# Optimization experiments

Hardware: AMD Instinct MI355X
Metric: run time of the kernel (lower is better)

The kernel has to match this reference:

```python
import jax, jax.numpy as jnp
import numpy as np

EPS = 1e-6
BASE_THETA = 10000.0


def setup_inputs() -> dict:
    key = jax.random.key(0)
    ks = jax.random.split(key, 6)
    S, E = 4096, 4096
    scale = 1.0 / np.sqrt(E)
    return {
        "x": jax.random.normal(ks[0], (S, E), dtype=jnp.float32),
        "w_q": jax.random.normal(ks[1], (E, E), dtype=jnp.float32) * scale,
        "w_k": jax.random.normal(ks[2], (E, E), dtype=jnp.float32) * scale,
        "w_v": jax.random.normal(ks[3], (E, E), dtype=jnp.float32) * scale,
        "w_out": jax.random.normal(ks[4], (E, E), dtype=jnp.float32) * scale,
        "scaling_factor": jax.random.uniform(ks[5], (E,), dtype=jnp.float32, minval=0.5, maxval=1.5),
    }


def _rope_apply(t, cos, sin):
    # t: (S, D) fp16; cos/sin: (S, D//2) fp16. Closed form of the per-position
    # block-diagonal 2x2 rotation matrix matmul in the original loop:
    # out[2j]   =  t[2j]*cos + t[2j+1]*sin
    # out[2j+1] = -t[2j]*sin + t[2j+1]*cos
    S, D = t.shape
    t2 = t.reshape(S, D // 2, 2)
    even, odd = t2[..., 0], t2[..., 1]
    out = jnp.stack([even * cos + odd * sin, -even * sin + odd * cos], axis=-1)
    return out.reshape(S, D)


def reference(x, w_q, w_k, w_v, w_out, scaling_factor):
    f16, f32 = jnp.float16, jnp.float32
    S, E = x.shape
    # __init__: q / q_inv / head rotations are identity; quantize = cast fp16 (scale 1).
    # q_inv * scaling_factor.view(1,-1) == diag(scaling_factor) -> row-scale weights.
    wq = (scaling_factor[:, None] * w_q).astype(f16)
    wk = (scaling_factor[:, None] * w_k).astype(f16)
    wv = (scaling_factor[:, None] * w_v).astype(f16)
    wo = w_out.astype(f16)

    # input @ identity; rms_norm in fp32
    xn = x * jax.lax.rsqrt(jnp.mean(x * x, axis=-1, keepdims=True) + EPS)
    xq = xn.astype(f16)

    # quantized matmuls: fp16 operands, fp32 accumulation, cast back to fp16
    q = (xq.astype(f32) @ wq.astype(f32)).astype(f16)
    k = (xq.astype(f32) @ wk.astype(f32)).astype(f16)
    v = (xq.astype(f32) @ wv.astype(f32)).astype(f16)

    # RoPE over full feature dim (size = E), vectorized over positions
    pos = jnp.arange(S, dtype=f32)[:, None]
    j = jnp.arange(E // 2, dtype=f32)[None, :]
    theta = pos / jnp.power(BASE_THETA, 2.0 * j / E)
    cos = jnp.cos(theta).astype(f16)
    sin = jnp.sin(theta).astype(f16)
    q = _rope_apply(q, cos, sin)
    k = _rope_apply(k, cos, sin)

    # rot_head_k_tiled is identity -> quantize is just fp16 cast (already fp16)
    scores = (q.astype(f32) @ k.T.astype(f32)).astype(f16)
    scores = scores / np.float16(np.sqrt(E))
    # causal mask: strict upper triangle -> -inf
    row = jnp.arange(S)[:, None]
    col = jnp.arange(S)[None, :]
    scores = jnp.where(col > row, jnp.float16(-jnp.inf), scores)
    attn_w = jax.nn.softmax(scores, axis=1)
    attn = attn_w @ v  # fp16 matmul as in original

    out = (attn.astype(f32) @ wo.astype(f32)).astype(f16)
    return out
```

## Files before the change

### kernel.cpp

```cpp
#include <hip/hip_runtime.h>
#include <hip/hip_bf16.h>
#include <cmath>


typedef _Float16 f16;
typedef _Float16 f16x4 __attribute__((ext_vector_type(4)));
typedef _Float16 f16x8 __attribute__((ext_vector_type(8)));
typedef float f32x4 __attribute__((ext_vector_type(4)));

#define S_DIM 4096
#define E_DIM 4096

__device__ __forceinline__ void gload_lds16(const void* g, void* l) {
  __builtin_amdgcn_global_load_lds((const __attribute__((address_space(1))) void*)g,
                                   (__attribute__((address_space(3))) void*)l,
                                   16, 0, 0);
}

__global__ __launch_bounds__(256) void rmsnorm_f16(const float* __restrict__ x,
                                                   f16* __restrict__ xq, int E) {
  const int row = blockIdx.x;
  const int t = threadIdx.x;
  const float4* xr = (const float4*)(x + (size_t)row * E);
  float4 v[4];
  float ss = 0.f;
#pragma unroll
  for (int i = 0; i < 4; ++i) {
    v[i] = xr[t + 256 * i];
    ss += v[i].x * v[i].x + v[i].y * v[i].y + v[i].z * v[i].z + v[i].w * v[i].w;
  }
#pragma unroll
  for (int o = 1; o < 64; o <<= 1) ss += __shfl_xor(ss, o);
  __shared__ float red[4];
  const int wid = t >> 6, lane = t & 63;
  if (lane == 0) red[wid] = ss;
  __syncthreads();
  const float tot = red[0] + red[1] + red[2] + red[3];
  const float r = 1.0f / sqrtf(tot / (float)E + 1e-6f);
  f16* xo = xq + (size_t)row * E;
#pragma unroll
  for (int i = 0; i < 4; ++i) {
    f16x4 o;
    o[0] = (f16)(v[i].x * r);
    o[1] = (f16)(v[i].y * r);
    o[2] = (f16)(v[i].z * r);
    o[3] = (f16)(v[i].w * r);
    *(f16x4*)(xo + 4 * (t + 256 * i)) = o;
  }
}

__global__ __launch_bounds__(256) void wconv_t(const float* __restrict__ W,
                                               const float* __restrict__ s,
                                               f16* __restrict__ WT, int N) {
  __shared__ f16 tile[64][65];
  const int tr = blockIdx.y * 64;
  const int tc = blockIdx.x * 64;
  const int t = threadIdx.x;
  const int r = t / 16;
  const int c4 = (t % 16) * 4;
#pragma unroll
  for (int i = 0; i < 4; ++i) {
    const int row = r + i * 16;
    float4 w = *(const float4*)(W + (size_t)(tr + row) * N + tc + c4);
    const float sc = s ? s[tr + row] : 1.0f;
    tile[row][c4 + 0] = (f16)(w.x * sc);
    tile[row][c4 + 1] = (f16)(w.y * sc);
    tile[row][c4 + 2] = (f16)(w.z * sc);
    tile[row][c4 + 3] = (f16)(w.w * sc);
  }
  __syncthreads();
#pragma unroll
  for (int i = 0; i < 4; ++i) {
    const int row = r + i * 16;
    f16x4 o;
    o[0] = tile[c4 + 0][row];
    o[1] = tile[c4 + 1][row];
    o[2] = tile[c4 + 2][row];
    o[3] = tile[c4 + 3][row];
    *(f16x4*)(WT + (size_t)(tc + row) * N + tr + c4) = o;
  }
}

__global__ __launch_bounds__(256) void freq_tab_k(float* __restrict__ tab) {
  const int j = blockIdx.x * 256 + threadIdx.x;
  if (j < 2048) tab[j] = (float)pow(10000.0, (double)j / 2048.0);
}

__global__ __launch_bounds__(256) void rope_qk(f16* __restrict__ q,
                                               f16* __restrict__ k,
                                               const float* __restrict__ ftab,
                                               int E) {
  const int idx = blockIdx.x * 256 + threadIdx.x;
  const int cpr = E / 8;
  const int pos = idx / cpr;
  const int ch = idx % cpr;
  const int j0 = ch * 4;
  const float fpos = (float)pos;
  f16x8 qv = *(f16x8*)(q + (size_t)idx * 8);
  f16x8 kv = *(f16x8*)(k + (size_t)idx * 8);
  f16x8 qo, ko;
#pragma unroll
  for (int p = 0; p < 4; ++p) {
    const int j = j0 + p;
    const float th = fpos / ftab[j];
    float sn, cs;
    sincosf(th, &sn, &cs);
    const f16 c16 = (f16)cs, s16 = (f16)sn;
    const float c = (float)c16, s = (float)s16;
    {
      const float e = (float)qv[2 * p], o = (float)qv[2 * p + 1];
      const f16 t1 = (f16)(e * c), t2 = (f16)(o * s);
      const f16 u1 = (f16)(-(e * s)), u2 = (f16)(o * c);
      qo[2 * p] = (f16)((float)t1 + (float)t2);
      qo[2 * p + 1] = (f16)((float)u1 + (float)u2);
    }
    {
      const float e = (float)kv[2 * p], o = (float)kv[2 * p + 1];
      const f16 t1 = (f16)(e * c), t2 = (f16)(o * s);
      const f16 u1 = (f16)(-(e * s)), u2 = (f16)(o * c);
      ko[2 * p] = (f16)((float)t1 + (float)t2);
      ko[2 * p + 1] = (f16)((float)u1 + (float)u2);
    }
  }
  *(f16x8*)(q + (size_t)idx * 8) = qo;
  *(f16x8*)(k + (size_t)idx * 8) = ko;
}

__global__ __launch_bounds__(256) void softmax_causal(f16* __restrict__ sc, int S) {
  const int row = blockIdx.x;
  const int t = threadIdx.x;
  f16* p = sc + (size_t)row * S;
  float v[16];
  bool msk[16];
#pragma unroll
  for (int i = 0; i < 2; ++i) {
    f16x8 a = *(const f16x8*)(p + (size_t)(i * 256 + t) * 8);
#pragma unroll
    for (int j = 0; j < 8; ++j) v[i * 8 + j] = (float)a[j];
  }
  float m = -1e30f;
#pragma unroll
  for (int i = 0; i < 2; ++i)
#pragma unroll
    for (int j = 0; j < 8; ++j) {
      const int col = (i * 256 + t) * 8 + j;
      const int ii = i * 8 + j;
      msk[ii] = (col > row);
      if (!msk[ii]) m = fmaxf(m, v[ii]);
    }
#pragma unroll
  for (int o = 1; o < 64; o <<= 1) m = fmaxf(m, __shfl_xor(m, o));
  __shared__ float red[4];
  const int wid = t >> 6, lane = t & 63;
  if (lane == 0) red[wid] = m;
  __syncthreads();
  m = fmaxf(fmaxf(red[0], red[1]), fmaxf(red[2], red[3]));
  __syncthreads();
  f16 e16[16];
  float sum = 0.f;
#pragma unroll
  for (int i = 0; i < 16; ++i) {
    if (msk[i]) {
      e16[i] = (f16)0.0f;
    } else {
      const f16 d16 = (f16)(v[i] - m);
      e16[i] = (f16)expf((float)d16);
      sum += (float)e16[i];
    }
  }
#pragma unroll
  for (int o = 1; o < 64; o <<= 1) sum += __shfl_xor(sum, o);
  if (lane == 0) red[wid] = sum;
  __syncthreads();
  sum = red[0] + red[1] + red[2] + red[3];
  const f16 den16 = (f16)sum;
  const float den = (float)den16;
#pragma unroll
  for (int i = 0; i < 2; ++i) {
    f16x8 o;
#pragma unroll
    for (int j = 0; j < 8; ++j) {
      const int ii = i * 8 + j;
      o[j] = msk[ii] ? (f16)0.0f : (f16)((float)e16[ii] / den);
    }
    *(f16x8*)(p + (size_t)(i * 256 + t) * 8) = o;
  }
}

__device__ __forceinline__ void store_out(f16* p, f16 v) { *p = v; }
__device__ __forceinline__ void store_out(float* p, f16 v) { *p = (float)v; }

template <typename OUT, int MODE>
__global__ __launch_bounds__(512, 2) void gemm256(const f16* __restrict__ A,
                                                  const f16* __restrict__ BT,
                                                  OUT* __restrict__ C,
                                                  int M, int N, int K, float alpha) {
  if (MODE == 1 && blockIdx.x > blockIdx.y) return;
  const int bm = blockIdx.y * 256, bn = blockIdx.x * 256;
  const int kend = (MODE == 2) ? (bm + 256 < K ? bm + 256 : K) : K;
  const int nt = kend >> 6;

  extern __shared__ char smem[];
  f16(*lds)[2][256][64] = (f16(*)[2][256][64])smem;

  const int tid = threadIdx.x;
  const int lane = tid & 63;
  const int wid = tid >> 6;
  const int wr = wid >> 2;
  const int wc = wid & 3;
  const f16* Ab = A + (size_t)bm * K;
  const f16* Bb = BT + (size_t)bn * K;

  const int l8 = lane >> 3;
  const int gxor8 = ((lane & 7) ^ l8) * 8;
  const int lr = lane & 15;
  const int shi = lane >> 4;
  const int rsw = lr & 7;

  auto STAGE_P = [&](int p) {
    const int c = p + 6;
    const int Ts = c >> 2, hh = c & 3;
    if (Ts >= nt) return;
    const int k0 = Ts << 6;
    const int bsel = Ts & 1;
#pragma unroll
    for (int l = 0; l < 2; ++l) {
      const int rih0 = wid * 16 + l * 8;
      if (hh == 0 || hh == 3) {
        const int row0 = (rih0 & 63) + ((rih0 >> 6) << 7) + ((hh == 3) ? 64 : 0);
        gload_lds16(Ab + (size_t)(row0 + l8) * K + k0 + gxor8,
                    &lds[bsel][0][row0][0]);
      } else {
        const int row0 = (rih0 & 31) + ((rih0 >> 5) << 6) + ((hh == 2) ? 32 : 0);
        gload_lds16(Bb + (size_t)(row0 + l8) * K + k0 + gxor8,
                    &lds[bsel][1][row0][0]);
      }
    }
  };

  f32x4 acc[8][4] = {};
  f16x8 afr0[4][2], afr1[4][2], b0r[2][2], b1r[2][2];

#pragma unroll
  for (int p = -6; p < 0; ++p) STAGE_P(p);

  for (int T = 0; T < nt; ++T) {
    const int cur = T & 1;
    __builtin_amdgcn_sched_barrier(0);
    if (T + 1 < nt) {
      asm volatile("s_waitcnt vmcnt(4)" ::: "memory");
    } else {
      asm volatile("s_waitcnt vmcnt(0)" ::: "memory");
    }
    __builtin_amdgcn_sched_barrier(0);
    __builtin_amdgcn_s_barrier();
    __builtin_amdgcn_sched_barrier(0);
#pragma unroll
    for (int m2 = 0; m2 < 4; ++m2)
#pragma unroll
      for (int kk = 0; kk < 2; ++kk)
        afr0[m2][kk] = *(const f16x8*)&lds[cur][0][wr * 128 + m2 * 16 + lr]
                                          [((kk * 4 + shi) ^ rsw) * 8];
#pragma unroll
    for (int n2 = 0; n2 < 2; ++n2)
#pragma unroll
      for (int kk = 0; kk < 2; ++kk)
        b0r[n2][kk] = *(const f16x8*)&lds[cur][1][wc * 64 + n2 * 16 + lr]
                                         [((kk * 4 + shi) ^ rsw) * 8];
    STAGE_P(4 * T);
    __builtin_amdgcn_sched_barrier(0);
    if (T > 0) {
      __builtin_amdgcn_s_setprio(1);
#pragma unroll
      for (int m2 = 0; m2 < 4; ++m2)
#pragma unroll
        for (int n2 = 0; n2 < 2; ++n2)
#pragma unroll
          for (int kk = 0; kk < 2; ++kk)
            acc[4 + m2][2 + n2] = __builtin_amdgcn_mfma_f32_16x16x32_f16(
                afr1[m2][kk], b1r[n2][kk], acc[4 + m2][2 + n2], 0, 0, 0);
      __builtin_amdgcn_s_setprio(0);
    }
    __builtin_amdgcn_sched_barrier(0);
#pragma unroll
    for (int n2 = 0; n2 < 2; ++n2)
#pragma unroll
      for (int kk = 0; kk < 2; ++kk)
        b1r[n2][kk] = *(const f16x8*)&lds[cur][1][wc * 64 + 32 + n2 * 16 + lr]
                                         [((kk * 4 + shi) ^ rsw) * 8];
    STAGE_P(4 * T + 1);
    __builtin_amdgcn_sched_barrier(0);
    __builtin_amdgcn_s_setprio(1);
#pragma unroll
    for (int m2 = 0; m2 < 4; ++m2)
#pragma unroll
      for (int n2 = 0; n2 < 2; ++n2)
#pragma unroll
        for (int kk = 0; kk < 2; ++kk)
          acc[m2][n2] = __builtin_amdgcn_mfma_f32_16x16x32_f16(
              afr0[m2][kk], b0r[n2][kk], acc[m2][n2], 0, 0, 0);
    __builtin_amdgcn_s_setprio(0);
    __builtin_amdgcn_sched_barrier(0);
    __builtin_amdgcn_s_barrier();
    __builtin_amdgcn_sched_barrier(0);
#pragma unroll
    for (int m2 = 0; m2 < 4; ++m2)
#pragma unroll
      for (int kk = 0; kk < 2; ++kk)
        afr1[m2][kk] = *(const f16x8*)&lds[cur][0][wr * 128 + 64 + m2 * 16 + lr]
                                          [((kk * 4 + shi) ^ rsw) * 8];
    STAGE_P(4 * T + 2);
    __builtin_amdgcn_sched_barrier(0);
    __builtin_amdgcn_s_setprio(1);
#pragma unroll
    for (int m2 = 0; m2 < 4; ++m2)
#pragma unroll
      for (int n2 = 0; n2 < 2; ++n2)
#pragma unroll
        for (int kk = 0; kk < 2; ++kk)
          acc[m2][2 + n2] = __builtin_amdgcn_mfma_f32_16x16x32_f16(
              afr0[m2][kk], b1r[n2][kk], acc[m2][2 + n2], 0, 0, 0);
    __builtin_amdgcn_s_setprio(0);
    __builtin_amdgcn_sched_barrier(0);
    STAGE_P(4 * T + 3);
    __builtin_amdgcn_sched_barrier(0);
    __builtin_amdgcn_s_setprio(1);
#pragma unroll
    for (int m2 = 0; m2 < 4; ++m2)
#pragma unroll
      for (int n2 = 0; n2 < 2; ++n2)
#pragma unroll
        for (int kk = 0; kk < 2; ++kk)
          acc[4 + m2][n2] = __builtin_amdgcn_mfma_f32_16x16x32_f16(
              afr1[m2][kk], b0r[n2][kk], acc[4 + m2][n2], 0, 0, 0);
    __builtin_amdgcn_s_setprio(0);
  }
  __builtin_amdgcn_s_setprio(1);
#pragma unroll
  for (int m2 = 0; m2 < 4; ++m2)
#pragma unroll
    for (int n2 = 0; n2 < 2; ++n2)
#pragma unroll
      for (int kk = 0; kk < 2; ++kk)
        acc[4 + m2][2 + n2] = __builtin_amdgcn_mfma_f32_16x16x32_f16(
            afr1[m2][kk], b1r[n2][kk], acc[4 + m2][2 + n2], 0, 0, 0);
  __builtin_amdgcn_s_setprio(0);

  const int rb_l = wr * 128 + (lane >> 4) * 4;
  const int cb_l = wc * 64 + (lane & 15);

  if (MODE == 4) {
    f16* tl = (f16*)smem;
    asm volatile("s_waitcnt lgkmcnt(0)" ::: "memory");
    __builtin_amdgcn_s_barrier();
#pragma unroll
    for (int mm = 0; mm < 8; ++mm)
#pragma unroll
      for (int nn = 0; nn < 4; ++nn) {
        const int c = cb_l + nn * 16;
#pragma unroll
        for (int r = 0; r < 4; ++r)
          tl[(size_t)c * 258 + rb_l + mm * 16 + r] = (f16)acc[mm][nn][r];
      }
    asm volatile("s_waitcnt lgkmcnt(0)" ::: "memory");
    __builtin_amdgcn_s_barrier();
    const int c = tid >> 1, hf = tid & 1;
#pragma unroll
    for (int i = 0; i < 16; ++i) {
      f16x8 v8 = *(const f16x8*)&tl[(size_t)c * 258 + hf * 128 + i * 8];
      *(f16x8*)((f16*)C + (size_t)(bn + c) * M + bm + hf * 128 + i * 8) = v8;
    }
    return;
  }

#pragma unroll
  for (int mm = 0; mm < 8; ++mm)
#pragma unroll
    for (int nn = 0; nn < 4; ++nn) {
      const int col = bn + cb_l + nn * 16;
#pragma unroll
      for (int r = 0; r < 4; ++r) {
        f16 h = (f16)acc[mm][nn][r];
        if (alpha != 1.0f) h = (f16)((float)h * alpha);
        store_out(&C[(size_t)(bm + rb_l + mm * 16 + r) * N + col], h);
      }
    }
}

extern "C" void kernel_launch(void* const* d_in, const int* in_sizes, int n_in,
                              void* d_out, int out_size, void* d_ws, size_t ws_size,
                              hipStream_t stream) {
  const float* x = (const float*)d_in[0];
  const float* wq = (const float*)d_in[1];
  const float* wk = (const float*)d_in[2];
  const float* wv = (const float*)d_in[3];
  const float* wo = (const float*)d_in[4];
  const float* sf = (const float*)d_in[5];
  float* out = (float*)d_out;

  const int S = S_DIM, E = E_DIM;
  const size_t U = (size_t)S * E * sizeof(f16);
  char* ws = (char*)d_ws;
  f16* xq = (f16*)(ws + 0 * U);
  f16* wT = (f16*)(ws + 1 * U);
  f16* q  = (f16*)(ws + 2 * U);
  f16* k  = (f16*)(ws + 3 * U);
  f16* vT = (f16*)d_out;

  const int LDSA = 131072;
  const int LDSB = 135168;
  hipFuncSetAttribute(reinterpret_cast<const void*>(&gemm256<f16, 0>),
                      hipFuncAttributeMaxDynamicSharedMemorySize, LDSA);
  hipFuncSetAttribute(reinterpret_cast<const void*>(&gemm256<f16, 1>),
                      hipFuncAttributeMaxDynamicSharedMemorySize, LDSA);
  hipFuncSetAttribute(reinterpret_cast<const void*>(&gemm256<f16, 2>),
                      hipFuncAttributeMaxDynamicSharedMemorySize, LDSA);
  hipFuncSetAttribute(reinterpret_cast<const void*>(&gemm256<f16, 4>),
                      hipFuncAttributeMaxDynamicSharedMemorySize, LDSB);
  hipFuncSetAttribute(reinterpret_cast<const void*>(&gemm256<float, 0>),
                      hipFuncAttributeMaxDynamicSharedMemorySize, LDSA);

  dim3 b256(256), b512(512);
  dim3 gT(E / 64, E / 64);
  dim3 gG(E / 256, S / 256);

  rmsnorm_f16<<<S, b256, 0, stream>>>(x, xq, E);

  wconv_t<<<gT, b256, 0, stream>>>(wq, sf, wT, E);
  gemm256<f16, 0><<<gG, b512, LDSA, stream>>>(xq, wT, q, S, E, E, 1.0f);
  wconv_t<<<gT, b256, 0, stream>>>(wk, sf, wT, E);
  gemm256<f16, 0><<<gG, b512, LDSA, stream>>>(xq, wT, k, S, E, E, 1.0f);
  wconv_t<<<gT, b256, 0, stream>>>(wv, sf, wT, E);
  gemm256<f16, 4><<<gG, b512, LDSB, stream>>>(xq, wT, vT, S, E, E, 1.0f);

  float* ftab = (float*)wT;
  freq_tab_k<<<8, b256, 0, stream>>>(ftab);
  rope_qk<<<(S * (E / 8)) / 256, b256, 0, stream>>>(q, k, ftab, E);

  f16* sc = wT;
  gemm256<f16, 1><<<dim3(S / 256, S / 256), b512, LDSA, stream>>>(q, k, sc, S, S,
                                                                  E, 1.0f / 64.0f);
  softmax_causal<<<S, b256, 0, stream>>>(sc, S);

  f16* attn = q;
  gemm256<f16, 2><<<gG, b512, LDSA, stream>>>(sc, vT, attn, S, E, S, 1.0f);

  f16* wT2 = k;
  wconv_t<<<gT, b256, 0, stream>>>(wo, (const float*)nullptr, wT2, E);
  gemm256<float, 0><<<gG, b512, LDSA, stream>>>(attn, wT2, out, S, E, E, 1.0f);
}
```

Before: 792.8 us.

## Unroll GEMM main loop by two with precomputed load pointers; trim causal softmax range

The GEMM main loop is rewritten as a templated per-tile step unrolled twice. Buffer indices become compile-time constants and global load addresses are precomputed pointers advanced by 64 each step, replacing the per-stage lambda's branchy index arithmetic. The causal softmax now skips loading, exponentiating and storing columns past the row's 256-aligned block, which the causal GEMM leaves unwritten. This assumes nt is even and at least 2, and leaves the skipped softmax columns as whatever the score buffer already holds.

```diff
diff --git a/kernel.cpp b/kernel.cpp
--- a/kernel.cpp
+++ b/kernel.cpp
@@ -130,24 +130,30 @@
   const int row = blockIdx.x;
   const int t = threadIdx.x;
   f16* p = sc + (size_t)row * S;
+  const int cend = (row & ~255) + 256;
   float v[16];
   bool msk[16];
+  bool act[2];
 #pragma unroll
   for (int i = 0; i < 2; ++i) {
-    f16x8 a = *(const f16x8*)(p + (size_t)(i * 256 + t) * 8);
-#pragma unroll
-    for (int j = 0; j < 8; ++j) v[i * 8 + j] = (float)a[j];
+    act[i] = ((i * 256 + t) * 8) < cend;
+    if (act[i]) {
+      f16x8 a = *(const f16x8*)(p + (size_t)(i * 256 + t) * 8);
+#pragma unroll
+      for (int j = 0; j < 8; ++j) v[i * 8 + j] = (float)a[j];
+    }
   }
   float m = -1e30f;
 #pragma unroll
   for (int i = 0; i < 2; ++i)
-#pragma unroll
-    for (int j = 0; j < 8; ++j) {
-      const int col = (i * 256 + t) * 8 + j;
-      const int ii = i * 8 + j;
-      msk[ii] = (col > row);
-      if (!msk[ii]) m = fmaxf(m, v[ii]);
-    }
+    if (act[i])
+#pragma unroll
+      for (int j = 0; j < 8; ++j) {
+        const int col = (i * 256 + t) * 8 + j;
+        const int ii = i * 8 + j;
+        msk[ii] = (col > row);
+        if (!msk[ii]) m = fmaxf(m, v[ii]);
+      }
 #pragma unroll
   for (int o = 1; o < 64; o <<= 1) m = fmaxf(m, __shfl_xor(m, o));
   __shared__ float red[4];
@@ -159,15 +165,19 @@
   f16 e16[16];
   float sum = 0.f;
 #pragma unroll
-  for (int i = 0; i < 16; ++i) {
-    if (msk[i]) {
-      e16[i] = (f16)0.0f;
-    } else {
-      const f16 d16 = (f16)(v[i] - m);
-      e16[i] = (f16)expf((float)d16);
-      sum += (float)e16[i];
-    }
-  }
+  for (int i = 0; i < 2; ++i)
+    if (act[i])
+#pragma unroll
+      for (int j = 0; j < 8; ++j) {
+        const int ii = i * 8 + j;
+        if (msk[ii]) {
+          e16[ii] = (f16)0.0f;
+        } else {
+          const f16 d16 = (f16)(v[ii] - m);
+          e16[ii] = (f16)expf((float)d16);
+          sum += (float)e16[ii];
+        }
+      }
 #pragma unroll
   for (int o = 1; o < 64; o <<= 1) sum += __shfl_xor(sum, o);
   if (lane == 0) red[wid] = sum;
@@ -177,6 +187,7 @@
   const float den = (float)den16;
 #pragma unroll
   for (int i = 0; i < 2; ++i) {
+    if (!act[i]) continue;
     f16x8 o;
 #pragma unroll
     for (int j = 0; j < 8; ++j) {
@@ -189,6 +200,121 @@
 
 __device__ __forceinline__ void store_out(f16* p, f16 v) { *p = v; }
 __device__ __forceinline__ void store_out(float* p, f16 v) { *p = (float)v; }
+
+#define MFMA_H __builtin_amdgcn_mfma_f32_16x16x32_f16
+
+template <int CURX, bool S01, bool S23, bool LASTV>
+__device__ __forceinline__ void tile_one(
+    f16 (*lds)[2][256][64], bool tailv, f32x4 (&acc)[8][4],
+    f16x8 (&afr0)[4][2], f16x8 (&afr1)[4][2], f16x8 (&b0r)[2][2],
+    f16x8 (&b1r)[2][2],
+    const f16*& gB2a, const f16*& gB2b, const f16*& gA3a, const f16*& gA3b,
+    const f16*& gA0a, const f16*& gA0b, const f16*& gB1a, const f16*& gB1b,
+    f16* dB2a, f16* dB2b, f16* dA3a, f16* dA3b,
+    f16* dA0a, f16* dA0b, f16* dB1a, f16* dB1b,
+    int wr, int wc, int lr, int shi, int rsw) {
+  __builtin_amdgcn_sched_barrier(0);
+  if (LASTV) {
+    asm volatile("s_waitcnt vmcnt(0)" ::: "memory");
+  } else {
+    asm volatile("s_waitcnt vmcnt(4)" ::: "memory");
+  }
+  __builtin_amdgcn_sched_barrier(0);
+  __builtin_amdgcn_s_barrier();
+  __builtin_amdgcn_sched_barrier(0);
+#pragma unroll
+  for (int m2 = 0; m2 < 4; ++m2)
+#pragma unroll
+    for (int kk = 0; kk < 2; ++kk)
+      afr0[m2][kk] = *(const f16x8*)&lds[CURX][0][wr * 128 + m2 * 16 + lr]
+                                        [((kk * 4 + shi) ^ rsw) * 8];
+#pragma unroll
+  for (int n2 = 0; n2 < 2; ++n2)
+#pragma unroll
+    for (int kk = 0; kk < 2; ++kk)
+      b0r[n2][kk] = *(const f16x8*)&lds[CURX][1][wc * 64 + n2 * 16 + lr]
+                                       [((kk * 4 + shi) ^ rsw) * 8];
+  if (S01) {
+    gload_lds16(gB2a, dB2a);
+    gload_lds16(gB2b, dB2b);
+  }
+  __builtin_amdgcn_sched_barrier(0);
+  if (tailv) {
+    __builtin_amdgcn_s_setprio(1);
+#pragma unroll
+    for (int m2 = 0; m2 < 4; ++m2)
+#pragma unroll
+      for (int n2 = 0; n2 < 2; ++n2)
+#pragma unroll
+        for (int kk = 0; kk < 2; ++kk)
+          acc[4 + m2][2 + n2] =
+              MFMA_H(afr1[m2][kk], b1r[n2][kk], acc[4 + m2][2 + n2], 0, 0, 0);
+    __builtin_amdgcn_s_setprio(0);
+  }
+  __builtin_amdgcn_sched_barrier(0);
+#pragma unroll
+  for (int n2 = 0; n2 < 2; ++n2)
+#pragma unroll
+    for (int kk = 0; kk < 2; ++kk)
+      b1r[n2][kk] = *(const f16x8*)&lds[CURX][1][wc * 64 + 32 + n2 * 16 + lr]
+                                       [((kk * 4 + shi) ^ rsw) * 8];
+  if (S01) {
+    gload_lds16(gA3a, dA3a);
+    gload_lds16(gA3b, dA3b);
+  }
+  __builtin_amdgcn_sched_barrier(0);
+  __builtin_amdgcn_s_setprio(1);
+#pragma unroll
+  for (int m2 = 0; m2 < 4; ++m2)
+#pragma unroll
+    for (int n2 = 0; n2 < 2; ++n2)
+#pragma unroll
+      for (int kk = 0; kk < 2; ++kk)
+        acc[m2][n2] = MFMA_H(afr0[m2][kk], b0r[n2][kk], acc[m2][n2], 0, 0, 0);
+  __builtin_amdgcn_s_setprio(0);
+  __builtin_amdgcn_sched_barrier(0);
+  __builtin_amdgcn_s_barrier();
+  __builtin_amdgcn_sched_barrier(0);
+#pragma unroll
+  for (int m2 = 0; m2 < 4; ++m2)
+#pragma unroll
+    for (int kk = 0; kk < 2; ++kk)
+      afr1[m2][kk] = *(const f16x8*)&lds[CURX][0][wr * 128 + 64 + m2 * 16 + lr]
+                                        [((kk * 4 + shi) ^ rsw) * 8];
+  if (S23) {
+    gload_lds16(gA0a, dA0a);
+    gload_lds16(gA0b, dA0b);
+  }
+  __builtin_amdgcn_sched_barrier(0);
+  __builtin_amdgcn_s_setprio(1);
+#pragma unroll
+  for (int m2 = 0; m2 < 4; ++m2)
+#pragma unroll
+    for (int n2 = 0; n2 < 2; ++n2)
+#pragma unroll
+      for (int kk = 0; kk < 2; ++kk)
+        acc[m2][2 + n2] =
+            MFMA_H(afr0[m2][kk], b1r[n2][kk], acc[m2][2 + n2], 0, 0, 0);
+  __builtin_amdgcn_s_setprio(0);
+  __builtin_amdgcn_sched_barrier(0);
+  if (S23) {
+    gload_lds16(gB1a, dB1a);
+    gload_lds16(gB1b, dB1b);
+  }
+  __builtin_amdgcn_sched_barrier(0);
+  __builtin_amdgcn_s_setprio(1);
+#pragma unroll
+  for (int m2 = 0; m2 < 4; ++m2)
+#pragma unroll
+    for (int n2 = 0; n2 < 2; ++n2)
+#pragma unroll
+      for (int kk = 0; kk < 2; ++kk)
+        acc[4 + m2][n2] =
+            MFMA_H(afr1[m2][kk], b0r[n2][kk], acc[4 + m2][n2], 0, 0, 0);
+  __builtin_amdgcn_s_setprio(0);
+  gB2a += 64; gB2b += 64; gA3a += 64; gA3b += 64;
+  gA0a += 64; gA0b += 64; gB1a += 64; gB1b += 64;
+}
 
 template <typename OUT, int MODE>
 __global__ __launch_bounds__(512, 2) void gemm256(const f16* __restrict__ A,
@@ -217,133 +343,88 @@
   const int shi = lane >> 4;
   const int rsw = lr & 7;
 
-  auto STAGE_P = [&](int p) {
-    const int c = p + 6;
-    const int Ts = c >> 2, hh = c & 3;
-    if (Ts >= nt) return;
-    const int k0 = Ts << 6;
-    const int bsel = Ts & 1;
-#pragma unroll
-    for (int l = 0; l < 2; ++l) {
-      const int rih0 = wid * 16 + l * 8;
-      if (hh == 0 || hh == 3) {
-        const int row0 = (rih0 & 63) + ((rih0 >> 6) << 7) + ((hh == 3) ? 64 : 0);
-        gload_lds16(Ab + (size_t)(row0 + l8) * K + k0 + gxor8,
-                    &lds[bsel][0][row0][0]);
-      } else {
-        const int row0 = (rih0 & 31) + ((rih0 >> 5) << 6) + ((hh == 2) ? 32 : 0);
-        gload_lds16(Bb + (size_t)(row0 + l8) * K + k0 + gxor8,
-                    &lds[bsel][1][row0][0]);
-      }
-    }
-  };
+  const int rih0 = wid * 16, rih1 = wid * 16 + 8;
+  const int a0r0 = (rih0 & 63) + ((rih0 >> 6) << 7);
+  const int a0r1 = (rih1 & 63) + ((rih1 >> 6) << 7);
+  const int a3r0 = a0r0 + 64, a3r1 = a0r1 + 64;
+  const int rB1_0 = (rih0 & 31) + ((rih0 >> 5) << 6);
+  const int rB1_1 = (rih1 & 31) + ((rih1 >> 5) << 6);
+  const int rB2_0 = rB1_0 + 32, rB2_1 = rB1_1 + 32;
+
+  gload_lds16(Ab + (size_t)(a0r0 + l8) * K + gxor8, &lds[0][0][a0r0][0]);
+  gload_lds16(Ab + (size_t)(a0r1 + l8) * K + gxor8, &lds[0][0][a0r1][0]);
+  gload_lds16(Bb + (size_t)(rB1_0 + l8) * K + gxor8, &lds[0][1][rB1_0][0]);
+  gload_lds16(Bb + (size_t)(rB1_1 + l8) * K + gxor8, &lds[0][1][rB1_1][0]);
+  gload_lds16(Bb + (size_t)(rB2_0 + l8) * K + gxor8, &lds[0][1][rB2_0][0]);
+  gload_lds16(Bb + (size_t)(rB2_1 + l8) * K + gxor8, &lds[0][1][rB2_1][0]);
+  gload_lds16(Ab + (size_t)(a3r0 + l8) * K + gxor8, &lds[0][0][a3r0][0]);
+  gload_lds16(Ab + (size_t)(a3r1 + l8) * K + gxor8, &lds[0][0][a3r1][0]);
+  gload_lds16(Ab + (size_t)(a0r0 + l8) * K + 64 + gxor8, &lds[1][0][a0r0][0]);
+  gload_lds16(Ab + (size_t)(a0r1 + l8) * K + 64 + gxor8, &lds[1][0][a0r1][0]);
+  gload_lds16(Bb + (size_t)(rB1_0 + l8) * K + 64 + gxor8, &lds[1][1][rB1_0][0]);
+  gload_lds16(Bb + (size_t)(rB1_1 + l8) * K + 64 + gxor8, &lds[1][1][rB1_1][0]);
+
+  const f16* gB2a = Bb + (size_t)(rB2_0 + l8) * K + 64 + gxor8;
+  const f16* gB2b = Bb + (size_t)(rB2_1 + l8) * K + 64 + gxor8;
+  const f16* gA3a = Ab + (size_t)(a3r0 + l8) * K + 64 + gxor8;
+  const f16* gA3b = Ab + (size_t)(a3r1 + l8) * K + 64 + gxor8;
+  const f16* gA0a = Ab + (size_t)(a0r0 + l8) * K + 128 + gxor8;
+  const f16* gA0b = Ab + (size_t)(a0r1 + l8) * K + 128 + gxor8;
+  const f16* gB1a = Bb + (size_t)(rB1_0 + l8) * K + 128 + gxor8;
+  const f16* gB1b = Bb + (size_t)(rB1_1 + l8) * K + 128 + gxor8;
+
+  f16* dA0[2][2];
+  f16* dA3[2][2];
+  f16* dB1[2][2];
+  f16* dB2[2][2];
+#pragma unroll
+  for (int b = 0; b < 2; ++b) {
+    dA0[b][0] = &lds[b][0][a0r0][0];
+    dA0[b][1] = &lds[b][0][a0r1][0];
+    dA3[b][0] = &lds[b][0][a3r0][0];
+    dA3[b][1] = &lds[b][0][a3r1][0];
+    dB1[b][0] = &lds[b][1][rB1_0][0];
+    dB1[b][1] = &lds[b][1][rB1_1][0];
+    dB2[b][0] = &lds[b][1][rB2_0][0];
+    dB2[b][1] = &lds[b][1][rB2_1][0];
+  }
 
   f32x4 acc[8][4] = {};
   f16x8 afr0[4][2], afr1[4][2], b0r[2][2], b1r[2][2];
 
-#pragma unroll
-  for (int p = -6; p < 0; ++p) STAGE_P(p);
-
-  for (int T = 0; T < nt; ++T) {
-    const int cur = T & 1;
-    __builtin_amdgcn_sched_barrier(0);
-    if (T + 1 < nt) {
-      asm volatile("s_waitcnt vmcnt(4)" ::: "memory");
-    } else {
-      asm volatile("s_waitcnt vmcnt(0)" ::: "memory");
-    }
-    __builtin_amdgcn_sched_barrier(0);
-    __builtin_amdgcn_s_barrier();
-    __builtin_amdgcn_sched_barrier(0);
-#pragma unroll
-    for (int m2 = 0; m2 < 4; ++m2)
+  bool first = true;
+  for (int T = 0; T < nt - 2; T += 2) {
+    tile_one<0, true, true, false>(lds, !first, acc, afr0, afr1, b0r, b1r,
+                                   gB2a, gB2b, gA3a, gA3b, gA0a, gA0b, gB1a, gB1b,
+                                   dB2[1][0], dB2[1][1], dA3[1][0], dA3[1][1],
+                                   dA0[0][0], dA0[0][1], dB1[0][0], dB1[0][1],
+                                   wr, wc, lr, shi, rsw);
+    first = false;
+    tile_one<1, true, true, false>(lds, true, acc, afr0, afr1, b0r, b1r,
+                                   gB2a, gB2b, gA3a, gA3b, gA0a, gA0b, gB1a, gB1b,
+                                   dB2[0][0], dB2[0][1], dA3[0][0], dA3[0][1],
+                                   dA0[1][0], dA0[1][1], dB1[1][0], dB1[1][1],
+                                   wr, wc, lr, shi, rsw);
+  }
+  tile_one<0, true, false, false>(lds, true, acc, afr0, afr1, b0r, b1r,
+                                  gB2a, gB2b, gA3a, gA3b, gA0a, gA0b, gB1a, gB1b,
+                                  dB2[1][0], dB2[1][1], dA3[1][0], dA3[1][1],
+                                  dA0[0][0], dA0[0][1], dB1[0][0], dB1[0][1],
+                                  wr, wc, lr, shi, rsw);
+  tile_one<1, false, false, true>(lds, true, acc, afr0, afr1, b0r, b1r,
+                                  gB2a, gB2b, gA3a, gA3b, gA0a, gA0b, gB1a, gB1b,
+                                  dB2[0][0], dB2[0][1], dA3[0][0], dA3[0][1],
+                                  dA0[1][0], dA0[1][1], dB1[1][0], dB1[1][1],
+                                  wr, wc, lr, shi, rsw);
+  __builtin_amdgcn_s_setprio(1);
+#pragma unroll
+  for (int m2 = 0; m2 < 4; ++m2)
+#pragma unroll
+    for (int n2 = 0; n2 < 2; ++n2)
 #pragma unroll
       for (int kk = 0; kk < 2; ++kk)
-        afr0[m2][kk] = *(const f16x8*)&lds[cur][0][wr * 128 + m2 * 16 + lr]
-                                          [((kk * 4 + shi) ^ rsw) * 8];
-#pragma unroll
-    for (int n2 = 0; n2 < 2; ++n2)
-#pragma unroll
-      for (int kk = 0; kk < 2; ++kk)
-        b0r[n2][kk] = *(const f16x8*)&lds[cur][1][wc * 64 + n2 * 16 + lr]
-                                         [((kk * 4 + shi) ^ rsw) * 8];
-    STAGE_P(4 * T);
-    __builtin_amdgcn_sched_barrier(0);
-    if (T > 0) {
-      __builtin_amdgcn_s_setprio(1);
-#pragma unroll
-      for (int m2 = 0; m2 < 4; ++m2)
-#pragma unroll
-        for (int n2 = 0; n2 < 2; ++n2)
-#pragma unroll
-          for (int kk = 0; kk < 2; ++kk)
-            acc[4 + m2][2 + n2] = __builtin_amdgcn_mfma_f32_16x16x32_f16(
-                afr1[m2][kk], b1r[n2][kk], acc[4 + m2][2 + n2], 0, 0, 0);
-      __builtin_amdgcn_s_setprio(0);
-    }
-    __builtin_amdgcn_sched_barrier(0);
-#pragma unroll
-    for (int n2 = 0; n2 < 2; ++n2)
-#pragma unroll
-      for (int kk = 0; kk < 2; ++kk)
-        b1r[n2][kk] = *(const f16x8*)&lds[cur][1][wc * 64 + 32 + n2 * 16 + lr]
-                                         [((kk * 4 + shi) ^ rsw) * 8];
-    STAGE_P(4 * T + 1);
-    __builtin_amdgcn_sched_barrier(0);
-    __builtin_amdgcn_s_setprio(1);
-#pragma unroll
-    for (int m2 = 0; m2 < 4; ++m2)
-#pragma unroll
-      for (int n2 = 0; n2 < 2; ++n2)
-#pragma unroll
-        for (int kk = 0; kk < 2; ++kk)
-          acc[m2][n2] = __builtin_amdgcn_mfma_f32_16x16x32_f16(
-              afr0[m2][kk], b0r[n2][kk], acc[m2][n2], 0, 0, 0);
-    __builtin_amdgcn_s_setprio(0);
-    __builtin_amdgcn_sched_barrier(0);
-    __builtin_amdgcn_s_barrier();
-    __builtin_amdgcn_sched_barrier(0);
-#pragma unroll
-    for (int m2 = 0; m2 < 4; ++m2)
-#pragma unroll
-      for (int kk = 0; kk < 2; ++kk)
-        afr1[m2][kk] = *(const f16x8*)&lds[cur][0][wr * 128 + 64 + m2 * 16 + lr]
-                                          [((kk * 4 + shi) ^ rsw) * 8];
-    STAGE_P(4 * T + 2);
-    __builtin_amdgcn_sched_barrier(0);
-    __builtin_amdgcn_s_setprio(1);
-#pragma unroll
-    for (int m2 = 0; m2 < 4; ++m2)
-#pragma unroll
-      for (int n2 = 0; n2 < 2; ++n2)
-#pragma unroll
-        for (int kk = 0; kk < 2; ++kk)
-          acc[m2][2 + n2] = __builtin_amdgcn_mfma_f32_16x16x32_f16(
-              afr0[m2][kk], b1r[n2][kk], acc[m2][2 + n2], 0, 0, 0);
-    __builtin_amdgcn_s_setprio(0);
-    __builtin_amdgcn_sched_barrier(0);
-    STAGE_P(4 * T + 3);
-    __builtin_amdgcn_sched_barrier(0);
-    __builtin_amdgcn_s_setprio(1);
-#pragma unroll
-    for (int m2 = 0; m2 < 4; ++m2)
-#pragma unroll
-      for (int n2 = 0; n2 < 2; ++n2)
-#pragma unroll
-        for (int kk = 0; kk < 2; ++kk)
-          acc[4 + m2][n2] = __builtin_amdgcn_mfma_f32_16x16x32_f16(
-              afr1[m2][kk], b0r[n2][kk], acc[4 + m2][n2], 0, 0, 0);
-    __builtin_amdgcn_s_setprio(0);
-  }
-  __builtin_amdgcn_s_setprio(1);
-#pragma unroll
-  for (int m2 = 0; m2 < 4; ++m2)
-#pragma unroll
-    for (int n2 = 0; n2 < 2; ++n2)
-#pragma unroll
-      for (int kk = 0; kk < 2; ++kk)
-        acc[4 + m2][2 + n2] = __builtin_amdgcn_mfma_f32_16x16x32_f16(
-            afr1[m2][kk], b1r[n2][kk], acc[4 + m2][2 + n2], 0, 0, 0);
+        acc[4 + m2][2 + n2] =
+            MFMA_H(afr1[m2][kk], b1r[n2][kk], acc[4 + m2][2 + n2], 0, 0, 0);
   __builtin_amdgcn_s_setprio(0);
 
   const int rb_l = wr * 128 + (lane >> 4) * 4;
```

Result: slower. 1.928 ms (+143.2%).
